# Optimization experiments

Measured on AMD Instinct MI355X. Metric: run time of the kernel, lower is better.

The kernel has to match this reference:

```python
import jax, jax.numpy as jnp
import numpy as np

HIDDEN = 1024
HEADS = 16
HEAD_DIM = HIDDEN // HEADS


def setup_inputs() -> dict:
    key = jax.random.key(0)
    ks = jax.random.split(key, 9)
    B, S = 4, 2048
    s = 1.0 / np.sqrt(HIDDEN)
    return {
        "inputs": jax.random.normal(ks[0], (B, S, HIDDEN), dtype=jnp.float32),
        "Wq": jax.random.normal(ks[1], (HIDDEN, HIDDEN), dtype=jnp.float32) * s,
        "bq": jnp.zeros((HIDDEN,), dtype=jnp.float32),
        "Wk": jax.random.normal(ks[2], (HIDDEN, HIDDEN), dtype=jnp.float32) * s,
        "bk": jnp.zeros((HIDDEN,), dtype=jnp.float32),
        "Wv": jax.random.normal(ks[3], (HIDDEN, HIDDEN), dtype=jnp.float32) * s,
        "bv": jnp.zeros((HIDDEN,), dtype=jnp.float32),
        "Wp": jax.random.normal(ks[4], (HIDDEN, HIDDEN), dtype=jnp.float32) * s,
        "bp": jnp.zeros((HIDDEN,), dtype=jnp.float32),
        "heads_z": jnp.ones((1, HEADS, 1, 1), dtype=jnp.float32),
        "hidden_z": jnp.ones((HIDDEN,), dtype=jnp.float32),
    }


def _split_heads(x):
    # [B,S,HIDDEN] -> [B,H,S,Dh]
    B, S, _ = x.shape
    return x.reshape(B, S, HEADS, HEAD_DIM).transpose(0, 2, 1, 3)


def reference(inputs, Wq, bq, Wk, bk, Wv, bv, Wp, bp, heads_z, hidden_z):
    q = _split_heads(inputs @ Wq.T + bq)
    k = _split_heads(inputs @ Wk.T + bk)
    v = _split_heads(inputs @ Wv.T + bv)
    scores = jnp.einsum("bhqd,bhkd->bhqk", q, k) / jnp.sqrt(
        jnp.asarray(HEAD_DIM, dtype=q.dtype))
    probs = jax.nn.softmax(scores, axis=-1)
    ctx = jnp.einsum("bhqk,bhkd->bhqd", probs, v)  # [B,H,S,Dh]
    ctx = ctx * heads_z
    B, H, S, D = ctx.shape
    ctx = ctx.transpose(0, 2, 1, 3).reshape(B, S, H * D)
    out = ctx @ Wp.T + bp
    out = out * hidden_z
    return out
```

## Files before the change

kernel.cpp:

```cpp
#include <hip/hip_runtime.h>
#include <hip/hip_bf16.h>

#define HID 1024
#define NH 16
#define DH 64
#define SEQ 2048
#define NB 4
#define MTOT (NB*SEQ)

typedef __attribute__((ext_vector_type(4))) float f32x4;
typedef __attribute__((ext_vector_type(16))) float f32x16;
typedef __attribute__((ext_vector_type(8))) __bf16 bf16x8;
typedef __attribute__((ext_vector_type(4))) __bf16 bf16x4;
typedef __attribute__((ext_vector_type(2))) __bf16 bf16x2;
typedef __attribute__((ext_vector_type(2))) int i32x2;

__device__ __forceinline__ f32x4 mfma16(bf16x8 a, bf16x8 b, f32x4 c) {
    return __builtin_amdgcn_mfma_f32_16x16x32_bf16(a, b, c, 0, 0, 0);
}
__device__ __forceinline__ f32x16 mfma32(bf16x8 a, bf16x8 b, f32x16 c) {
    return __builtin_amdgcn_mfma_f32_32x32x16_bf16(a, b, c, 0, 0, 0);
}

__device__ __forceinline__ void gload16(const void* g, void* l) {
    __builtin_amdgcn_global_load_lds(
        (const __attribute__((address_space(1))) unsigned int*)g,
        (__attribute__((address_space(3))) unsigned int*)l, 16, 0, 0);
}

__device__ __forceinline__ float fexp2(float x) {
#if __has_builtin(__builtin_amdgcn_exp2f)
    return __builtin_amdgcn_exp2f(x);
#else
    return exp2f(x);
#endif
}

__device__ __forceinline__ unsigned pkbf2(float lo, float hi) {
    union { bf16x2 v; unsigned u; } c;
    c.v = (bf16x2){ (__bf16)lo, (__bf16)hi };
    return c.u;
}

__device__ __forceinline__ void swap32(unsigned &a, unsigned &b) {
#if __has_builtin(__builtin_amdgcn_permlane32_swap)
    i32x2 r = __builtin_amdgcn_permlane32_swap((int)a, (int)b, false, false);
    a = (unsigned)r.x; b = (unsigned)r.y;
#else
    const bool hi = (threadIdx.x & 32) != 0;
    unsigned ta = __shfl_xor(a, 32), tb = __shfl_xor(b, 32);
    unsigned na = hi ? tb : a;
    unsigned nb = hi ? b : ta;
    a = na; b = nb;
#endif
}

__device__ __forceinline__ float swapmaxf(float x) {
    unsigned a = __float_as_uint(x), b = a;
    swap32(a, b);
    return fmaxf(__uint_as_float(a), __uint_as_float(b));
}
__device__ __forceinline__ float swapaddf(float x) {
    unsigned a = __float_as_uint(x), b = a;
    swap32(a, b);
    return __uint_as_float(a) + __uint_as_float(b);
}

__global__ __launch_bounds__(256)
void cvt5(const float* __restrict__ X,  const float* __restrict__ Wq,
          const float* __restrict__ Wk, const float* __restrict__ Wv,
          const float* __restrict__ Wp,
          __bf16* __restrict__ Xb,  __bf16* __restrict__ Wqb,
          __bf16* __restrict__ Wkb, __bf16* __restrict__ Wvb,
          __bf16* __restrict__ Wpb)
{
    const float* src; __bf16* dst; int n;
    switch (blockIdx.y) {
        case 0:  src = X;  dst = Xb;  n = MTOT * HID; break;
        case 1:  src = Wq; dst = Wqb; n = HID * HID;  break;
        case 2:  src = Wk; dst = Wkb; n = HID * HID;  break;
        case 3:  src = Wv; dst = Wvb; n = HID * HID;  break;
        default: src = Wp; dst = Wpb; n = HID * HID;  break;
    }
    const int stride = gridDim.x * 256 * 4;
    for (int i = (blockIdx.x * 256 + threadIdx.x) * 4; i < n; i += stride) {
        float4 v = *(const float4*)(src + i);
        bf16x4 o = { (__bf16)v.x, (__bf16)v.y, (__bf16)v.z, (__bf16)v.w };
        *(bf16x4*)(dst + i) = o;
    }
}

__global__ __launch_bounds__(256)
void gemm_qkv(const __bf16* __restrict__ A,
              const __bf16* __restrict__ Wq, const __bf16* __restrict__ Wk,
              const __bf16* __restrict__ Wv,
              const float* __restrict__ bq, const float* __restrict__ bk,
              const float* __restrict__ bv,
              __bf16* __restrict__ Qo, __bf16* __restrict__ Ko, __bf16* __restrict__ Vo)
{
    __shared__ __bf16 As[128 * 32];
    __shared__ __bf16 Bs[128 * 32];
    const int mode = blockIdx.z;
    const __bf16* W    = mode == 0 ? Wq : mode == 1 ? Wk : Wv;
    const float*  bias = mode == 0 ? bq : mode == 1 ? bk : bv;
    __bf16*       Og   = mode == 0 ? Qo : mode == 1 ? Ko : Vo;

    const int tid  = threadIdx.x;
    const int lane = tid & 63, wid = tid >> 6;
    const int m0 = blockIdx.x * 128;
    const int n0 = blockIdx.y * 128;
    const int wm = (wid >> 1) * 64, wn = (wid & 1) * 64;

    f32x4 acc[4][4];
    #pragma unroll
    for (int i = 0; i < 4; i++)
        #pragma unroll
        for (int j = 0; j < 4; j++) acc[i][j] = (f32x4){0.f, 0.f, 0.f, 0.f};

    for (int kt = 0; kt < HID; kt += 32) {
        #pragma unroll
        for (int i = 0; i < 2; i++) {
            int c = wid * 128 + i * 64 + lane;
            int row = c >> 2, slot = c & 3;
            int ss = slot ^ (row & 3);
            gload16(A + (size_t)(m0 + row) * HID + kt + ss * 8, (char*)As + c * 16);
            gload16(W + (size_t)(n0 + row) * HID + kt + ss * 8, (char*)Bs + c * 16);
        }
        __syncthreads();

        bf16x8 af[4], bfr[4];
        #pragma unroll
        for (int mi = 0; mi < 4; mi++) {
            int row = wm + mi * 16 + (lane & 15);
            int off = row * 64 + (((lane >> 4) * 16) ^ ((row & 3) << 4));
            af[mi] = *(const bf16x8*)((const char*)As + off);
        }
        #pragma unroll
        for (int ni = 0; ni < 4; ni++) {
            int row = wn + ni * 16 + (lane & 15);
            int off = row * 64 + (((lane >> 4) * 16) ^ ((row & 3) << 4));
            bfr[ni] = *(const bf16x8*)((const char*)Bs + off);
        }
        #pragma unroll
        for (int mi = 0; mi < 4; mi++)
            #pragma unroll
            for (int ni = 0; ni < 4; ni++)
                acc[mi][ni] = mfma16(af[mi], bfr[ni], acc[mi][ni]);
        __syncthreads();
    }

    #pragma unroll
    for (int mi = 0; mi < 4; mi++)
        #pragma unroll
        for (int ni = 0; ni < 4; ni++)
            #pragma unroll
            for (int r = 0; r < 4; r++) {
                int m = m0 + wm + mi * 16 + ((lane >> 4) * 4) + r;
                int n = n0 + wn + ni * 16 + (lane & 15);
                float v = acc[mi][ni][r] + bias[n];
                int b = m >> 11, s = m & (SEQ - 1);
                int h = n >> 6,  d = n & 63;
                size_t idx;
                if (mode == 2) idx = ((size_t)(b * NH + h) * DH + d) * SEQ + s;
                else           idx = ((size_t)(b * NH + h) * SEQ + s) * DH + d;
                Og[idx] = (__bf16)v;
            }
}

__global__ __launch_bounds__(256)
void gemm_proj(const __bf16* __restrict__ A, const __bf16* __restrict__ W,
               const float* __restrict__ bias, const float* __restrict__ hz,
               float* __restrict__ outp)
{
    __shared__ __bf16 As[128 * 32];
    __shared__ __bf16 Bs[128 * 32];
    const int tid  = threadIdx.x;
    const int lane = tid & 63, wid = tid >> 6;
    const int m0 = blockIdx.x * 128;
    const int n0 = blockIdx.y * 128;
    const int wm = (wid >> 1) * 64, wn = (wid & 1) * 64;

    f32x4 acc[4][4];
    #pragma unroll
    for (int i = 0; i < 4; i++)
        #pragma unroll
        for (int j = 0; j < 4; j++) acc[i][j] = (f32x4){0.f, 0.f, 0.f, 0.f};

    for (int kt = 0; kt < HID; kt += 32) {
        #pragma unroll
        for (int i = 0; i < 2; i++) {
            int c = wid * 128 + i * 64 + lane;
            int row = c >> 2, slot = c & 3;
            int ss = slot ^ (row & 3);
            gload16(A + (size_t)(m0 + row) * HID + kt + ss * 8, (char*)As + c * 16);
            gload16(W + (size_t)(n0 + row) * HID + kt + ss * 8, (char*)Bs + c * 16);
        }
        __syncthreads();

        bf16x8 af[4], bfr[4];
        #pragma unroll
        for (int mi = 0; mi < 4; mi++) {
            int row = wm + mi * 16 + (lane & 15);
            int off = row * 64 + (((lane >> 4) * 16) ^ ((row & 3) << 4));
            af[mi] = *(const bf16x8*)((const char*)As + off);
        }
        #pragma unroll
        for (int ni = 0; ni < 4; ni++) {
            int row = wn + ni * 16 + (lane & 15);
            int off = row * 64 + (((lane >> 4) * 16) ^ ((row & 3) << 4));
            bfr[ni] = *(const bf16x8*)((const char*)Bs + off);
        }
        #pragma unroll
        for (int mi = 0; mi < 4; mi++)
            #pragma unroll
            for (int ni = 0; ni < 4; ni++)
                acc[mi][ni] = mfma16(af[mi], bfr[ni], acc[mi][ni]);
        __syncthreads();
    }

    #pragma unroll
    for (int mi = 0; mi < 4; mi++)
        #pragma unroll
        for (int ni = 0; ni < 4; ni++)
            #pragma unroll
            for (int r = 0; r < 4; r++) {
                int m = m0 + wm + mi * 16 + ((lane >> 4) * 4) + r;
                int n = n0 + wn + ni * 16 + (lane & 15);
                outp[(size_t)m * HID + n] = (acc[mi][ni][r] + bias[n]) * hz[n];
            }
}

#define KVB 128
#define SM_SCALE 0.18033688f

__global__ __launch_bounds__(512, 4)
void attn(const __bf16* __restrict__ Q, const __bf16* __restrict__ K,
          const __bf16* __restrict__ VT, const float* __restrict__ heads_z,
          __bf16* __restrict__ C)
{
    __shared__ __bf16 Ks[2][KVB * 64];
    __shared__ __bf16 Vs[2][64 * KVB];
    const int tid = threadIdx.x, lane = tid & 63, wid = tid >> 6;
    const int lh = lane >> 5;
    const int id = blockIdx.x;
    const int bh = (id & 7) | ((id >> 6) << 3);
    const int qb = (id >> 3) & 7;
    const int b = bh >> 4, hd = bh & 15;
    const __bf16* Qg = Q + (size_t)bh * SEQ * DH;
    const __bf16* Kg = K + (size_t)bh * SEQ * DH;
    const __bf16* Vg = VT + (size_t)bh * DH * SEQ;
    const int q = qb * 256 + wid * 32 + (lane & 31);
    const int r0 = lane & 31;
    const int kx = (r0 & 7) << 4;
    const int vx = (r0 & 15) << 4;

    bf16x8 qf[4];
    #pragma unroll
    for (int s = 0; s < 4; s++)
        qf[s] = *(const bf16x8*)(Qg + (size_t)q * DH + s * 16 + lh * 8);

    f32x16 ctx0, ctx1;
    #pragma unroll
    for (int r = 0; r < 16; r++) { ctx0[r] = 0.f; ctx1[r] = 0.f; }
    float mrun = -1e30f, lrun = 0.f;

    const int kr0 = tid >> 3,          ksl0 = tid & 7,          kss0 = ksl0 ^ (kr0 & 7);
    const int kr1 = (tid + 512) >> 3,  ksl1 = tid & 7,          kss1 = ksl1 ^ (kr1 & 7);
    const int vr0 = tid >> 4,          vsl0 = tid & 15,         vss0 = vsl0 ^ (vr0 & 15);
    const int vr1 = (tid + 512) >> 4,  vsl1 = tid & 15,         vss1 = vsl1 ^ (vr1 & 15);

    {
        gload16(Kg + (size_t)kr0 * DH + kss0 * 8, (char*)&Ks[0][0] + tid * 16);
        gload16(Kg + (size_t)kr1 * DH + kss1 * 8, (char*)&Ks[0][0] + (tid + 512) * 16);
        gload16(Vg + (size_t)vr0 * SEQ + 0 + vss0 * 8, (char*)&Vs[0][0] + tid * 16);
        gload16(Vg + (size_t)vr1 * SEQ + 0 + vss1 * 8, (char*)&Vs[0][0] + (tid + 512) * 16);
    }
    __syncthreads();

    int cur = 0;
    for (int kv0 = 0; kv0 < SEQ; kv0 += KVB) {
        if (kv0 + KVB < SEQ) {
            int nx = kv0 + KVB;
            gload16(Kg + (size_t)(nx + kr0) * DH + kss0 * 8, (char*)&Ks[cur ^ 1][0] + tid * 16);
            gload16(Kg + (size_t)(nx + kr1) * DH + kss1 * 8, (char*)&Ks[cur ^ 1][0] + (tid + 512) * 16);
            gload16(Vg + (size_t)vr0 * SEQ + nx + vss0 * 8, (char*)&Vs[cur ^ 1][0] + tid * 16);
            gload16(Vg + (size_t)vr1 * SEQ + nx + vss1 * 8, (char*)&Vs[cur ^ 1][0] + (tid + 512) * 16);
        }

        #pragma unroll
        for (int hh = 0; hh < 2; hh++) {
            const char* Kb = (const char*)&Ks[cur][0] + hh * 64 * 128;
            const char* Vb = (const char*)&Vs[cur][0];

            f32x16 st0, st1;
            #pragma unroll
            for (int r = 0; r < 16; r++) { st0[r] = 0.f; st1[r] = 0.f; }
            __builtin_amdgcn_s_setprio(1);
            #pragma unroll
            for (int s = 0; s < 4; s++) {
                int co = (2 * s + lh) << 4;
                bf16x8 k0 = *(const bf16x8*)(Kb + r0 * 128 + (co ^ kx));
                bf16x8 k1 = *(const bf16x8*)(Kb + (r0 + 32) * 128 + (co ^ kx));
                st0 = mfma32(k0, qf[s], st0);
                st1 = mfma32(k1, qf[s], st1);
            }
            __builtin_amdgcn_s_setprio(0);

            float t8[8];
            #pragma unroll
            for (int j = 0; j < 8; j++)
                t8[j] = fmaxf(fmaxf(st0[2 * j], st0[2 * j + 1]),
                              fmaxf(st1[2 * j], st1[2 * j + 1]));
            float t4a = fmaxf(t8[0], t8[1]), t4b = fmaxf(t8[2], t8[3]);
            float t4c = fmaxf(t8[4], t8[5]), t4d = fmaxf(t8[6], t8[7]);
            float pm = fmaxf(fmaxf(t4a, t4b), fmaxf(t4c, t4d));
            pm = swapmaxf(pm);
            pm *= SM_SCALE;
            if (!__all(pm <= mrun + 8.f)) {
                float nm = fmaxf(mrun, pm);
                float al = fexp2(mrun - nm);
                lrun *= al; mrun = nm;
                #pragma unroll
                for (int r = 0; r < 16; r++) { ctx0[r] *= al; ctx1[r] *= al; }
            }
            const float mneg = -mrun;
            float rsA = 0.f, rsB = 0.f, rsC = 0.f, rsD = 0.f;
            #pragma unroll
            for (int r = 0; r < 16; r += 2) {
                float e0 = fexp2(fmaf(st0[r],     SM_SCALE, mneg));
                float e1 = fexp2(fmaf(st0[r + 1], SM_SCALE, mneg));
                float e2 = fexp2(fmaf(st1[r],     SM_SCALE, mneg));
                float e3 = fexp2(fmaf(st1[r + 1], SM_SCALE, mneg));
                st0[r] = e0; st0[r + 1] = e1; st1[r] = e2; st1[r + 1] = e3;
                rsA += e0; rsB += e1; rsC += e2; rsD += e3;
            }
            lrun += swapaddf((rsA + rsB) + (rsC + rsD));

            unsigned X0 = pkbf2(st0[0],  st0[1]),  X1 = pkbf2(st0[2],  st0[3]);
            unsigned X2 = pkbf2(st0[4],  st0[5]),  X3 = pkbf2(st0[6],  st0[7]);
            unsigned X4 = pkbf2(st0[8],  st0[9]),  X5 = pkbf2(st0[10], st0[11]);
            unsigned X6 = pkbf2(st0[12], st0[13]), X7 = pkbf2(st0[14], st0[15]);
            unsigned Y0 = pkbf2(st1[0],  st1[1]),  Y1 = pkbf2(st1[2],  st1[3]);
            unsigned Y2 = pkbf2(st1[4],  st1[5]),  Y3 = pkbf2(st1[6],  st1[7]);
            unsigned Y4 = pkbf2(st1[8],  st1[9]),  Y5 = pkbf2(st1[10], st1[11]);
            unsigned Y6 = pkbf2(st1[12], st1[13]), Y7 = pkbf2(st1[14], st1[15]);
            swap32(X0, X2); swap32(X1, X3);
            swap32(X4, X6); swap32(X5, X7);
            swap32(Y0, Y2); swap32(Y1, Y3);
            swap32(Y4, Y6); swap32(Y5, Y7);
            union W4 { unsigned w[4]; bf16x8 v; };
            W4 pf[4];
            pf[0].w[0]=X0; pf[0].w[1]=X1; pf[0].w[2]=X2; pf[0].w[3]=X3;
            pf[1].w[0]=X4; pf[1].w[1]=X5; pf[1].w[2]=X6; pf[1].w[3]=X7;
            pf[2].w[0]=Y0; pf[2].w[1]=Y1; pf[2].w[2]=Y2; pf[2].w[3]=Y3;
            pf[3].w[0]=Y4; pf[3].w[1]=Y5; pf[3].w[2]=Y6; pf[3].w[3]=Y7;

            __builtin_amdgcn_s_setprio(1);
            #pragma unroll
            for (int s = 0; s < 4; s++) {
                int co = (hh * 8 + 2 * s + lh) << 4;
                bf16x8 v0 = *(const bf16x8*)(Vb + r0 * 256 + (co ^ vx));
                bf16x8 v1 = *(const bf16x8*)(Vb + (r0 + 32) * 256 + (co ^ vx));
                ctx0 = mfma32(v0, pf[s].v, ctx0);
                ctx1 = mfma32(v1, pf[s].v, ctx1);
            }
            __builtin_amdgcn_s_setprio(0);
        }

        __syncthreads();
        cur ^= 1;
    }

    const float hzv = heads_z[hd];
    const float rl = hzv / lrun;
    __bf16* Crow = C + (size_t)(b * SEQ + q) * HID + hd * DH;
    #pragma unroll
    for (int g = 0; g < 4; g++) {
        bf16x4 o0, o1;
        #pragma unroll
        for (int j = 0; j < 4; j++) {
            o0[j] = (__bf16)(ctx0[4 * g + j] * rl);
            o1[j] = (__bf16)(ctx1[4 * g + j] * rl);
        }
        int d0 = 8 * g + 4 * lh;
        *(bf16x4*)(Crow + d0) = o0;
        *(bf16x4*)(Crow + 32 + d0) = o1;
    }
}

extern "C" void kernel_launch(void* const* d_in, const int* in_sizes, int n_in,
                              void* d_out, int out_size, void* d_ws, size_t ws_size,
                              hipStream_t stream)
{
    const float* X    = (const float*)d_in[0];
    const float* Wq   = (const float*)d_in[1];
    const float* bq   = (const float*)d_in[2];
    const float* Wk   = (const float*)d_in[3];
    const float* bk   = (const float*)d_in[4];
    const float* Wv   = (const float*)d_in[5];
    const float* bv   = (const float*)d_in[6];
    const float* Wp   = (const float*)d_in[7];
    const float* bp   = (const float*)d_in[8];
    const float* hz   = (const float*)d_in[9];
    const float* hidz = (const float*)d_in[10];

    __bf16* ws  = (__bf16*)d_ws;
    __bf16* Xb  = ws;
    __bf16* Wqb = Xb  + (size_t)MTOT * HID;
    __bf16* Wkb = Wqb + (size_t)HID * HID;
    __bf16* Wvb = Wkb + (size_t)HID * HID;
    __bf16* Wpb = Wvb + (size_t)HID * HID;
    __bf16* Qb  = Wpb + (size_t)HID * HID;
    __bf16* Kb  = Qb  + (size_t)MTOT * HID;
    __bf16* VTb = Kb  + (size_t)MTOT * HID;
    __bf16* Cb  = VTb + (size_t)MTOT * HID;

    cvt5<<<dim3(2048, 5), 256, 0, stream>>>(X, Wq, Wk, Wv, Wp, Xb, Wqb, Wkb, Wvb, Wpb);

    gemm_qkv<<<dim3(MTOT / 128, HID / 128, 3), 256, 0, stream>>>(
        Xb, Wqb, Wkb, Wvb, bq, bk, bv, Qb, Kb, VTb);

    attn<<<dim3(512), 512, 0, stream>>>(Qb, Kb, VTb, hz, Cb);

    gemm_proj<<<dim3(MTOT / 128, HID / 128), 256, 0, stream>>>(Cb, Wpb, bp, hidz, (float*)d_out);
}
```

Measured before the change: 209.7 us.

## Fold softmax scale into Q, compute row sums with MFMA, lighten max reduction

The QKV GEMM epilogue now multiplies Q by the softmax scale, so the attention loop drops the per-element fma with the scale. The V store is vectorised to 4-wide bf16 writes. In the attention kernel the row-max uses 3-input max trees that fold in the running max. The cross-half lane swap now runs only when a rescale is needed. The row sum of the exponentials is computed by an extra MFMA against a ones vector instead of VALU adds plus a swap. This trades VALU work for extra matrix-core instructions and rounds the pre-scaled Q to bf16.

```diff
diff --git a/kernel.cpp b/kernel.cpp
--- a/kernel.cpp
+++ b/kernel.cpp
@@ -7,6 +7,7 @@
 #define SEQ 2048
 #define NB 4
 #define MTOT (NB*SEQ)
+#define SM_SCALE 0.18033688f
 
 typedef __attribute__((ext_vector_type(4))) float f32x4;
 typedef __attribute__((ext_vector_type(16))) float f32x16;
@@ -41,6 +42,8 @@
     c.v = (bf16x2){ (__bf16)lo, (__bf16)hi };
     return c.u;
 }
+
+#define F3(a,b,c) fmaxf(fmaxf((a),(b)),(c))
 
 __device__ __forceinline__ void swap32(unsigned &a, unsigned &b) {
 #if __has_builtin(__builtin_amdgcn_permlane32_swap)
@@ -59,11 +62,6 @@
     unsigned a = __float_as_uint(x), b = a;
     swap32(a, b);
     return fmaxf(__uint_as_float(a), __uint_as_float(b));
-}
-__device__ __forceinline__ float swapaddf(float x) {
-    unsigned a = __float_as_uint(x), b = a;
-    swap32(a, b);
-    return __uint_as_float(a) + __uint_as_float(b);
 }
 
 __global__ __launch_bounds__(256)
@@ -103,7 +101,6 @@
     const int mode = blockIdx.z;
     const __bf16* W    = mode == 0 ? Wq : mode == 1 ? Wk : Wv;
     const float*  bias = mode == 0 ? bq : mode == 1 ? bk : bv;
-    __bf16*       Og   = mode == 0 ? Qo : mode == 1 ? Ko : Vo;
 
     const int tid  = threadIdx.x;
     const int lane = tid & 63, wid = tid >> 6;
@@ -149,22 +146,37 @@
         __syncthreads();
     }
 
-    #pragma unroll
-    for (int mi = 0; mi < 4; mi++)
-        #pragma unroll
-        for (int ni = 0; ni < 4; ni++)
-            #pragma unroll
-            for (int r = 0; r < 4; r++) {
-                int m = m0 + wm + mi * 16 + ((lane >> 4) * 4) + r;
+    if (mode == 2) {
+        #pragma unroll
+        for (int mi = 0; mi < 4; mi++)
+            #pragma unroll
+            for (int ni = 0; ni < 4; ni++) {
+                int m = m0 + wm + mi * 16 + ((lane >> 4) * 4);
                 int n = n0 + wn + ni * 16 + (lane & 15);
-                float v = acc[mi][ni][r] + bias[n];
                 int b = m >> 11, s = m & (SEQ - 1);
                 int h = n >> 6,  d = n & 63;
-                size_t idx;
-                if (mode == 2) idx = ((size_t)(b * NH + h) * DH + d) * SEQ + s;
-                else           idx = ((size_t)(b * NH + h) * SEQ + s) * DH + d;
-                Og[idx] = (__bf16)v;
-            }
+                bf16x4 o;
+                #pragma unroll
+                for (int r = 0; r < 4; r++) o[r] = (__bf16)(acc[mi][ni][r] + bias[n]);
+                *(bf16x4*)(Vo + ((size_t)(b * NH + h) * DH + d) * SEQ + s) = o;
+            }
+    } else {
+        const float qs = (mode == 0) ? SM_SCALE : 1.0f;
+        __bf16* Og = (mode == 0) ? Qo : Ko;
+        #pragma unroll
+        for (int mi = 0; mi < 4; mi++)
+            #pragma unroll
+            for (int ni = 0; ni < 4; ni++)
+                #pragma unroll
+                for (int r = 0; r < 4; r++) {
+                    int m = m0 + wm + mi * 16 + ((lane >> 4) * 4) + r;
+                    int n = n0 + wn + ni * 16 + (lane & 15);
+                    float v = (acc[mi][ni][r] + bias[n]) * qs;
+                    int b = m >> 11, s = m & (SEQ - 1);
+                    int h = n >> 6,  d = n & 63;
+                    Og[((size_t)(b * NH + h) * SEQ + s) * DH + d] = (__bf16)v;
+                }
+    }
 }
 
 __global__ __launch_bounds__(256)
@@ -231,7 +243,6 @@
 }
 
 #define KVB 128
-#define SM_SCALE 0.18033688f
 
 __global__ __launch_bounds__(512, 4)
 void attn(const __bf16* __restrict__ Q, const __bf16* __restrict__ K,
@@ -254,6 +265,10 @@
     const int kx = (r0 & 7) << 4;
     const int vx = (r0 & 15) << 4;
 
+    bf16x8 ones8;
+    #pragma unroll
+    for (int j = 0; j < 8; j++) ones8[j] = (__bf16)1.0f;
+
     bf16x8 qf[4];
     #pragma unroll
     for (int s = 0; s < 4; s++)
@@ -264,17 +279,15 @@
     for (int r = 0; r < 16; r++) { ctx0[r] = 0.f; ctx1[r] = 0.f; }
     float mrun = -1e30f, lrun = 0.f;
 
-    const int kr0 = tid >> 3,          ksl0 = tid & 7,          kss0 = ksl0 ^ (kr0 & 7);
-    const int kr1 = (tid + 512) >> 3,  ksl1 = tid & 7,          kss1 = ksl1 ^ (kr1 & 7);
-    const int vr0 = tid >> 4,          vsl0 = tid & 15,         vss0 = vsl0 ^ (vr0 & 15);
-    const int vr1 = (tid + 512) >> 4,  vsl1 = tid & 15,         vss1 = vsl1 ^ (vr1 & 15);
-
-    {
-        gload16(Kg + (size_t)kr0 * DH + kss0 * 8, (char*)&Ks[0][0] + tid * 16);
-        gload16(Kg + (size_t)kr1 * DH + kss1 * 8, (char*)&Ks[0][0] + (tid + 512) * 16);
-        gload16(Vg + (size_t)vr0 * SEQ + 0 + vss0 * 8, (char*)&Vs[0][0] + tid * 16);
-        gload16(Vg + (size_t)vr1 * SEQ + 0 + vss1 * 8, (char*)&Vs[0][0] + (tid + 512) * 16);
-    }
+    const int kr0 = tid >> 3,          kss0 = (tid & 7) ^ (kr0 & 7);
+    const int kr1 = (tid + 512) >> 3,  kss1 = (tid & 7) ^ (kr1 & 7);
+    const int vr0 = tid >> 4,          vss0 = (tid & 15) ^ (vr0 & 15);
+    const int vr1 = (tid + 512) >> 4,  vss1 = (tid & 15) ^ (vr1 & 15);
+
+    gload16(Kg + (size_t)kr0 * DH + kss0 * 8, (char*)&Ks[0][0] + tid * 16);
+    gload16(Kg + (size_t)kr1 * DH + kss1 * 8, (char*)&Ks[0][0] + (tid + 512) * 16);
+    gload16(Vg + (size_t)vr0 * SEQ + 0 + vss0 * 8, (char*)&Vs[0][0] + tid * 16);
+    gload16(Vg + (size_t)vr1 * SEQ + 0 + vss1 * 8, (char*)&Vs[0][0] + (tid + 512) * 16);
     __syncthreads();
 
     int cur = 0;
@@ -306,17 +319,25 @@
             }
             __builtin_amdgcn_s_setprio(0);
 
-            float t8[8];
-            #pragma unroll
-            for (int j = 0; j < 8; j++)
-                t8[j] = fmaxf(fmaxf(st0[2 * j], st0[2 * j + 1]),
-                              fmaxf(st1[2 * j], st1[2 * j + 1]));
-            float t4a = fmaxf(t8[0], t8[1]), t4b = fmaxf(t8[2], t8[3]);
-            float t4c = fmaxf(t8[4], t8[5]), t4d = fmaxf(t8[6], t8[7]);
-            float pm = fmaxf(fmaxf(t4a, t4b), fmaxf(t4c, t4d));
-            pm = swapmaxf(pm);
-            pm *= SM_SCALE;
-            if (!__all(pm <= mrun + 8.f)) {
+            float l1[11];
+            l1[0] = F3(st0[0],  st0[1],  st0[2]);
+            l1[1] = F3(st0[3],  st0[4],  st0[5]);
+            l1[2] = F3(st0[6],  st0[7],  st0[8]);
+            l1[3] = F3(st0[9],  st0[10], st0[11]);
+            l1[4] = F3(st0[12], st0[13], st0[14]);
+            l1[5] = F3(st0[15], st1[0],  st1[1]);
+            l1[6] = F3(st1[2],  st1[3],  st1[4]);
+            l1[7] = F3(st1[5],  st1[6],  st1[7]);
+            l1[8] = F3(st1[8],  st1[9],  st1[10]);
+            l1[9] = F3(st1[11], st1[12], st1[13]);
+            l1[10] = fmaxf(st1[14], st1[15]);
+            float l2a = F3(l1[0], l1[1], l1[2]);
+            float l2b = F3(l1[3], l1[4], l1[5]);
+            float l2c = F3(l1[6], l1[7], l1[8]);
+            float l2d = fmaxf(l1[9], l1[10]);
+            float pml = F3(F3(l2a, l2b, l2c), l2d, mrun) - 0.f;
+            if (!__all(pml <= mrun + 8.f)) {
+                float pm = swapmaxf(pml);
                 float nm = fmaxf(mrun, pm);
                 float al = fexp2(mrun - nm);
                 lrun *= al; mrun = nm;
@@ -324,17 +345,11 @@
                 for (int r = 0; r < 16; r++) { ctx0[r] *= al; ctx1[r] *= al; }
             }
             const float mneg = -mrun;
-            float rsA = 0.f, rsB = 0.f, rsC = 0.f, rsD = 0.f;
-            #pragma unroll
-            for (int r = 0; r < 16; r += 2) {
-                float e0 = fexp2(fmaf(st0[r],     SM_SCALE, mneg));
-                float e1 = fexp2(fmaf(st0[r + 1], SM_SCALE, mneg));
-                float e2 = fexp2(fmaf(st1[r],     SM_SCALE, mneg));
-                float e3 = fexp2(fmaf(st1[r + 1], SM_SCALE, mneg));
-                st0[r] = e0; st0[r + 1] = e1; st1[r] = e2; st1[r + 1] = e3;
-                rsA += e0; rsB += e1; rsC += e2; rsD += e3;
-            }
-            lrun += swapaddf((rsA + rsB) + (rsC + rsD));
+            #pragma unroll
+            for (int r = 0; r < 16; r++) {
+                st0[r] = fexp2(st0[r] + mneg);
+                st1[r] = fexp2(st1[r] + mneg);
+            }
 
             unsigned X0 = pkbf2(st0[0],  st0[1]),  X1 = pkbf2(st0[2],  st0[3]);
             unsigned X2 = pkbf2(st0[4],  st0[5]),  X3 = pkbf2(st0[6],  st0[7]);
@@ -355,6 +370,10 @@
             pf[2].w[0]=Y0; pf[2].w[1]=Y1; pf[2].w[2]=Y2; pf[2].w[3]=Y3;
             pf[3].w[0]=Y4; pf[3].w[1]=Y5; pf[3].w[2]=Y6; pf[3].w[3]=Y7;
 
+            st0[0] = 0.f;
+            #pragma unroll
+            for (int s = 0; s < 4; s++) st0 = mfma32(ones8, pf[s].v, st0);
+
             __builtin_amdgcn_s_setprio(1);
             #pragma unroll
             for (int s = 0; s < 4; s++) {
@@ -365,6 +384,8 @@
                 ctx1 = mfma32(v1, pf[s].v, ctx1);
             }
             __builtin_amdgcn_s_setprio(0);
+
+            lrun += st0[0];
         }
 
         __syncthreads();
```

Result: faster. 197.2 us (-5.9%).
